# Kernel optimization log

Measured on AMD Instinct MI355X. Metric: run time of the kernel, lower is better.

## Reference

```python
import jax, jax.numpy as jnp
import numpy as np

U, I, D, OUT = 8192, 16384, 64, 64

def setup_inputs() -> dict:
    key = jax.random.key(0)
    k1, k2, k3, k4 = jax.random.split(key, 4)
    user_emb = jax.random.normal(k1, (U, D), dtype=jnp.float32)
    item_emb = jax.random.normal(k2, (I, D), dtype=jnp.float32)
    attention_weight = jax.random.normal(k3, (D, OUT), dtype=jnp.float32) * (1.0 / np.sqrt(D))
    adj_matrix = jax.random.randint(k4, (U, I), 0, 2, dtype=jnp.int32)
    return {"user_emb": user_emb, "item_emb": item_emb,
            "attention_weight": attention_weight, "adj_matrix": adj_matrix}

def reference(user_emb, item_emb, attention_weight, adj_matrix):
    # score[u,i] = <user_emb[u], item_emb[i]>  (torch.inner)
    score = jnp.einsum('ud,id->ui', user_emb, item_emb)
    # mask non-edges to 0 (NOT -inf, faithful to torch.where(adj>0, score, 0))
    score = jnp.where(adj_matrix > 0, score, 0.0)
    score = jax.nn.softmax(score, axis=1)
    # flag == True path: aggregate items into users, then project
    output = score @ item_emb          # [U, D]
    output = output @ attention_weight  # [U, OUT]
    return output
```

## Files before the change

kernel.cpp:

```cpp
#include <hip/hip_runtime.h>
#include <hip/hip_bf16.h>
#include <math.h>

#define U_N   8192
#define I_N   16384
#define D_N   64
#define OUT_N 64
#define BN    32
#define NCH   16
#define ITERS 32
#define VN_ST 72
#define VT_ST 40

typedef _Float16 half8  __attribute__((ext_vector_type(8)));
typedef short    bf16x8 __attribute__((ext_vector_type(8)));
typedef short    bf16x4 __attribute__((ext_vector_type(4)));
typedef float    f32x4  __attribute__((ext_vector_type(4)));
typedef int      int4v  __attribute__((ext_vector_type(4)));

static __device__ __forceinline__ unsigned short f2bf(float f) {
    union { __hip_bfloat16 h; unsigned short u; } cv;
    cv.h = __float2bfloat16(f);
    return cv.u;
}
static __device__ __forceinline__ void bar() {
    asm volatile("s_waitcnt lgkmcnt(0)\n\ts_barrier" ::: "memory");
}
static __device__ __forceinline__ f32x4 pv_mfma(bf16x4 a, bf16x4 b, f32x4 c) {
#if __has_builtin(__builtin_amdgcn_mfma_f32_16x16x16bf16_1k)
    return __builtin_amdgcn_mfma_f32_16x16x16bf16_1k(a, b, c, 0, 0, 0);
#else
    f32x4 d;
    asm volatile("v_mfma_f32_16x16x16_bf16 %0, %1, %2, %3"
                 : "=v"(d) : "v"(a), "v"(b), "v"(c));
    return d;
#endif
}

__global__ __launch_bounds__(256)
void prep_items(const float* __restrict__ item,
                _Float16* __restrict__ itemH,
                unsigned short* __restrict__ itemTt)
{
    const int i = blockIdx.x * 256 + threadIdx.x;
    const float* src = item + (size_t)i * D_N;
    f32x4 v[16];
    #pragma unroll
    for (int j = 0; j < 16; ++j) v[j] = *(const f32x4*)(src + 4 * j);

    #pragma unroll
    for (int j = 0; j < 8; ++j) {
        half8 h;
        #pragma unroll
        for (int k = 0; k < 4; ++k) { h[k] = (_Float16)v[2*j][k]; h[4+k] = (_Float16)v[2*j+1][k]; }
        *(half8*)&itemH[(size_t)i * D_N + 8 * j] = h;
    }
    const size_t tb = (size_t)(i >> 5) * (D_N * 32) + (i & 31);
    #pragma unroll
    for (int d = 0; d < 64; ++d)
        itemTt[tb + (size_t)d * 32] = f2bf(v[d >> 2][d & 3]);
}

#define DECL_SET(S) \
    int4v adj##S##a, adj##S##b; \
    half8 vn##S; bf16x8 vt##S;

#define LOAD_ADJ(S, tidx) do { \
    const size_t o_ = (size_t)(tidx) * BN; \
    adj##S##a = *(const int4v*)&adjq[o_];      \
    adj##S##b = *(const int4v*)&adjq[o_ + 16]; \
} while (0)

#define LOAD_TILE(S, tidx) do { \
    const size_t o_ = (size_t)(tidx) * BN; \
    vn##S = *(const half8*)&itemH[(ibase0 + o_ + (t >> 3)) * D_N + (t & 7) * 8]; \
    vt##S = *(const bf16x8*)&itemTt[((ibase0 + o_) >> 5) * (D_N * 32) \
                                    + (size_t)(t >> 2) * 32 + (t & 3) * 8]; \
} while (0)

#define COMMIT(S, bufw) do { \
    *(half8*)&Vn[bufw][(t >> 3) * VN_ST + (t & 7) * 8] = vn##S; \
    *(bf16x8*)&Vt[bufw][(t >> 2) * VT_ST + (t & 3) * 8] = vt##S; \
} while (0)

#define MASKS(S, ma, mb) \
    const unsigned ma = ((adj##S##a[0] != 0) ? 1u : 0u) | ((adj##S##a[1] != 0) ? 2u : 0u) | \
                        ((adj##S##a[2] != 0) ? 4u : 0u) | ((adj##S##a[3] != 0) ? 8u : 0u); \
    const unsigned mb = ((adj##S##b[0] != 0) ? 1u : 0u) | ((adj##S##b[1] != 0) ? 2u : 0u) | \
                        ((adj##S##b[2] != 0) ? 4u : 0u) | ((adj##S##b[3] != 0) ? 8u : 0u);

#define COMPUTE_REST(ma, mb, bufr) do { \
    half8 a00 = *(const half8*)&Vn[bufr][(c)      * VN_ST      + q * 8]; \
    half8 a01 = *(const half8*)&Vn[bufr][(c)      * VN_ST + 32 + q * 8]; \
    half8 a10 = *(const half8*)&Vn[bufr][(16 + c) * VN_ST      + q * 8]; \
    half8 a11 = *(const half8*)&Vn[bufr][(16 + c) * VN_ST + 32 + q * 8]; \
    f32x4 T0 = (f32x4){0.f,0.f,0.f,0.f}; \
    f32x4 T1 = (f32x4){0.f,0.f,0.f,0.f}; \
    T0 = __builtin_amdgcn_mfma_f32_16x16x32_f16(a00, ufrag0, T0, 0, 0, 0); \
    T0 = __builtin_amdgcn_mfma_f32_16x16x32_f16(a01, ufrag1, T0, 0, 0, 0); \
    T1 = __builtin_amdgcn_mfma_f32_16x16x32_f16(a10, ufrag0, T1, 0, 0, 0); \
    T1 = __builtin_amdgcn_mfma_f32_16x16x32_f16(a11, ufrag1, T1, 0, 0, 0); \
    bf16x4 p0, p1; \
    float e_; \
    e_ = __expf(((ma) & 1u) ? T0[0] : 0.0f); p0[0] = (short)f2bf(e_); lc += e_; \
    e_ = __expf(((ma) & 2u) ? T0[1] : 0.0f); p0[1] = (short)f2bf(e_); lc += e_; \
    e_ = __expf(((ma) & 4u) ? T0[2] : 0.0f); p0[2] = (short)f2bf(e_); lc += e_; \
    e_ = __expf(((ma) & 8u) ? T0[3] : 0.0f); p0[3] = (short)f2bf(e_); lc += e_; \
    e_ = __expf(((mb) & 1u) ? T1[0] : 0.0f); p1[0] = (short)f2bf(e_); lc += e_; \
    e_ = __expf(((mb) & 2u) ? T1[1] : 0.0f); p1[1] = (short)f2bf(e_); lc += e_; \
    e_ = __expf(((mb) & 4u) ? T1[2] : 0.0f); p1[2] = (short)f2bf(e_); lc += e_; \
    e_ = __expf(((mb) & 8u) ? T1[3] : 0.0f); p1[3] = (short)f2bf(e_); lc += e_; \
    bf16x4 vb00 = *(const bf16x4*)&Vt[bufr][(c)      * VT_ST      + 4 * q]; \
    bf16x4 vb01 = *(const bf16x4*)&Vt[bufr][(c)      * VT_ST + 16 + 4 * q]; \
    bf16x4 vb10 = *(const bf16x4*)&Vt[bufr][(16 + c) * VT_ST      + 4 * q]; \
    bf16x4 vb11 = *(const bf16x4*)&Vt[bufr][(16 + c) * VT_ST + 16 + 4 * q]; \
    bf16x4 vb20 = *(const bf16x4*)&Vt[bufr][(32 + c) * VT_ST      + 4 * q]; \
    bf16x4 vb21 = *(const bf16x4*)&Vt[bufr][(32 + c) * VT_ST + 16 + 4 * q]; \
    bf16x4 vb30 = *(const bf16x4*)&Vt[bufr][(48 + c) * VT_ST      + 4 * q]; \
    bf16x4 vb31 = *(const bf16x4*)&Vt[bufr][(48 + c) * VT_ST + 16 + 4 * q]; \
    O0 = pv_mfma(p0, vb00, O0);  O0 = pv_mfma(p1, vb01, O0); \
    O1 = pv_mfma(p0, vb10, O1);  O1 = pv_mfma(p1, vb11, O1); \
    O2 = pv_mfma(p0, vb20, O2);  O2 = pv_mfma(p1, vb21, O2); \
    O3 = pv_mfma(p0, vb30, O3);  O3 = pv_mfma(p1, vb31, O3); \
} while (0)

__global__ __launch_bounds__(256, 4)
void atten_main(const float* __restrict__ user_emb,
                const _Float16* __restrict__ itemH,
                const unsigned short* __restrict__ itemTt,
                const int*   __restrict__ adj,
                float* __restrict__ wsO,
                float* __restrict__ wsL)
{
    __shared__ _Float16 Vn[2][BN * VN_ST];
    __shared__ short    Vt[2][D_N * VT_ST];

    const int ch   = blockIdx.x;
    const int ub   = blockIdx.y;
    const int t    = threadIdx.x;
    const int w    = t >> 6;
    const int lane = t & 63;
    const int c    = lane & 15;
    const int q    = lane >> 4;

    const int    urow0  = ub * 64 + w * 16;
    const size_t ibase0 = (size_t)ch * (I_N / NCH);

    half8 ufrag0, ufrag1;
    {
        const float* up = user_emb + (size_t)(urow0 + c) * D_N + q * 8;
        f32x4 a0 = *(const f32x4*)(up);
        f32x4 b0 = *(const f32x4*)(up + 4);
        f32x4 a1 = *(const f32x4*)(up + 32);
        f32x4 b1 = *(const f32x4*)(up + 36);
        #pragma unroll
        for (int j = 0; j < 4; ++j) {
            ufrag0[j] = (_Float16)a0[j]; ufrag0[4 + j] = (_Float16)b0[j];
            ufrag1[j] = (_Float16)a1[j]; ufrag1[4 + j] = (_Float16)b1[j];
        }
    }

    f32x4 O0 = (f32x4){0.f,0.f,0.f,0.f};
    f32x4 O1 = O0, O2 = O0, O3 = O0;
    float lc = 0.f;

    const int* adjq = adj + (size_t)(urow0 + c) * I_N + ibase0 + 4 * q;

    DECL_SET(A)
    DECL_SET(B)

    LOAD_TILE(A, 0); LOAD_ADJ(A, 0);
    LOAD_TILE(B, 1); LOAD_ADJ(B, 1);
    COMMIT(A, 0);
    LOAD_TILE(A, 2);
    bar();

    for (int k = 0; k < ITERS; k += 2) {
        {
            MASKS(A, ma, mb)
            COMMIT(B, 1);
            const int ia = (k + 2 < ITERS) ? k + 2 : ITERS - 1;
            const int iv = (k + 3 < ITERS) ? k + 3 : ITERS - 1;
            LOAD_ADJ(A, ia);
            LOAD_TILE(B, iv);
            COMPUTE_REST(ma, mb, 0);
            bar();
        }
        {
            MASKS(B, ma, mb)
            COMMIT(A, 0);
            const int ia = (k + 3 < ITERS) ? k + 3 : ITERS - 1;
            const int iv = (k + 4 < ITERS) ? k + 4 : ITERS - 1;
            LOAD_ADJ(B, ia);
            LOAD_TILE(A, iv);
            COMPUTE_REST(ma, mb, 1);
            bar();
        }
    }

    lc += __shfl_xor(lc, 16);
    lc += __shfl_xor(lc, 32);

    {
        float* d0 = wsO + ((size_t)ch * U_N + urow0 + 4 * q + 0) * D_N;
        float* d1 = wsO + ((size_t)ch * U_N + urow0 + 4 * q + 1) * D_N;
        float* d2 = wsO + ((size_t)ch * U_N + urow0 + 4 * q + 2) * D_N;
        float* d3 = wsO + ((size_t)ch * U_N + urow0 + 4 * q + 3) * D_N;
        d0[c] = O0[0]; d0[16 + c] = O1[0]; d0[32 + c] = O2[0]; d0[48 + c] = O3[0];
        d1[c] = O0[1]; d1[16 + c] = O1[1]; d1[32 + c] = O2[1]; d1[48 + c] = O3[1];
        d2[c] = O0[2]; d2[16 + c] = O1[2]; d2[32 + c] = O2[2]; d2[48 + c] = O3[2];
        d3[c] = O0[3]; d3[16 + c] = O1[3]; d3[32 + c] = O2[3]; d3[48 + c] = O3[3];
    }
    if (q == 0)
        wsL[(size_t)ch * U_N + urow0 + c] = lc;
}

__global__ __launch_bounds__(256)
void atten_combine(const float* __restrict__ wsO,
                   const float* __restrict__ wsL,
                   const float* __restrict__ attw,
                   float* __restrict__ out,
                   int nch)
{
    __shared__ float inv[64];
    __shared__ float agg[64][68];
    __shared__ float Wl[64][68];

    const int t  = threadIdx.x;
    const int u0 = blockIdx.x * 64;

    {
        const int d = t >> 2, o0 = (t & 3) * 16;
        const float* src = attw + d * OUT_N + o0;
        #pragma unroll
        for (int j = 0; j < 4; ++j)
            *(f32x4*)&Wl[d][o0 + 4 * j] = *(const f32x4*)(src + 4 * j);
    }
    if (t < 64) {
        float L = 0.f;
        for (int cc = 0; cc < nch; ++cc) L += wsL[(size_t)cc * U_N + u0 + t];
        inv[t] = 1.0f / L;
    }
    __syncthreads();

    {
        const int ul = t >> 2, d0 = (t & 3) * 16;
        const int u = u0 + ul;
        f32x4 a4[4];
        #pragma unroll
        for (int j = 0; j < 4; ++j) a4[j] = (f32x4){0.f, 0.f, 0.f, 0.f};
        for (int cc = 0; cc < nch; ++cc) {
            const float* src = wsO + ((size_t)cc * U_N + u) * D_N + d0;
            #pragma unroll
            for (int j = 0; j < 4; ++j) a4[j] += *(const f32x4*)(src + 4 * j);
        }
        const float s = inv[ul];
        #pragma unroll
        for (int j = 0; j < 4; ++j)
            *(f32x4*)&agg[ul][d0 + 4 * j] = a4[j] * s;
    }
    __syncthreads();

    {
        const int ul = t >> 2, o0 = (t & 3) * 16;
        f32x4 acc[4];
        #pragma unroll
        for (int j = 0; j < 4; ++j) acc[j] = (f32x4){0.f, 0.f, 0.f, 0.f};
        for (int d = 0; d < 64; ++d) {
            const float av = agg[ul][d];
            #pragma unroll
            for (int j = 0; j < 4; ++j) {
                f32x4 wv = *(const f32x4*)&Wl[d][o0 + 4 * j];
                acc[j] += wv * av;
            }
        }
        float* dst = out + (size_t)(u0 + ul) * OUT_N + o0;
        #pragma unroll
        for (int j = 0; j < 4; ++j)
            *(f32x4*)(dst + 4 * j) = acc[j];
    }
}

extern "C" void kernel_launch(void* const* d_in, const int* in_sizes, int n_in,
                              void* d_out, int out_size, void* d_ws, size_t ws_size,
                              hipStream_t stream)
{
    const float* user_emb = (const float*)d_in[0];
    const float* item_emb = (const float*)d_in[1];
    const float* attw     = (const float*)d_in[2];
    const int*   adj      = (const int*)d_in[3];
    float* out = (float*)d_out;

    float*          wsO    = (float*)d_ws;
    float*          wsL    = wsO + (size_t)NCH * U_N * D_N;
    _Float16*       itemH  = (_Float16*)(wsL + (size_t)NCH * U_N);
    unsigned short* itemTt = (unsigned short*)(itemH + (size_t)I_N * D_N);

    prep_items<<<dim3(I_N / 256), 256, 0, stream>>>(item_emb, itemH, itemTt);
    atten_main<<<dim3(NCH, U_N / 64), 256, 0, stream>>>(user_emb, itemH, itemTt, adj,
                                                        wsO, wsL);
    atten_combine<<<dim3(U_N / 64), 256, 0, stream>>>(wsO, wsL, attw, out, NCH);
}
```

Measured before the change: 740.7 us.

## Use exp2 with prescaled user rows, truncating bf16 pack, and wider Vt reads

User fragments are prescaled by log2(e) so the softmax can use the hardware exp2 instruction directly. Probabilities are packed to bf16 by truncation with a byte-permute instead of round-to-nearest conversion. The transposed item layout is permuted so each lane reads one 16-byte Vt vector instead of two 8-byte ones. Mask bitfields are dropped in favour of reading the adj vectors directly, and the adj loads move after the compute so the registers can be reused. The item-chunk split is halved (NCH 8, more iterations per block), which halves the partial-output workspace and the reduction work but also halves the grid size.

```diff
diff --git a/kernel.cpp b/kernel.cpp
--- a/kernel.cpp
+++ b/kernel.cpp
@@ -7,8 +7,8 @@
 #define D_N   64
 #define OUT_N 64
 #define BN    32
-#define NCH   16
-#define ITERS 32
+#define NCH   8
+#define ITERS 64
 #define VN_ST 72
 #define VT_ST 40
 
@@ -22,6 +22,24 @@
     union { __hip_bfloat16 h; unsigned short u; } cv;
     cv.h = __float2bfloat16(f);
     return cv.u;
+}
+static __device__ __forceinline__ float fast_exp2(float x) {
+#if __has_builtin(__builtin_amdgcn_exp2f)
+    return __builtin_amdgcn_exp2f(x);
+#else
+    return __expf(x * 0.6931471805599453f);
+#endif
+}
+static __device__ __forceinline__ bf16x4 pack4(float a, float b, float c2, float d) {
+    union { unsigned u[2]; bf16x4 h; } x;
+#if __has_builtin(__builtin_amdgcn_perm)
+    x.u[0] = __builtin_amdgcn_perm(__float_as_uint(b), __float_as_uint(a), 0x07060302u);
+    x.u[1] = __builtin_amdgcn_perm(__float_as_uint(d), __float_as_uint(c2), 0x07060302u);
+#else
+    x.u[0] = (__float_as_uint(b) & 0xffff0000u) | (__float_as_uint(a) >> 16);
+    x.u[1] = (__float_as_uint(d) & 0xffff0000u) | (__float_as_uint(c2) >> 16);
+#endif
+    return x.h;
 }
 static __device__ __forceinline__ void bar() {
     asm volatile("s_waitcnt lgkmcnt(0)\n\ts_barrier" ::: "memory");
@@ -55,7 +73,9 @@
         for (int k = 0; k < 4; ++k) { h[k] = (_Float16)v[2*j][k]; h[4+k] = (_Float16)v[2*j+1][k]; }
         *(half8*)&itemH[(size_t)i * D_N + 8 * j] = h;
     }
-    const size_t tb = (size_t)(i >> 5) * (D_N * 32) + (i & 31);
+    const int il    = i & 31;
+    const int islot = 8 * ((il & 15) >> 2) + ((il >> 4) << 2) + (il & 3);
+    const size_t tb = (size_t)(i >> 5) * (D_N * 32) + islot;
     #pragma unroll
     for (int d = 0; d < 64; ++d)
         itemTt[tb + (size_t)d * 32] = f2bf(v[d >> 2][d & 3]);
@@ -83,45 +103,44 @@
     *(bf16x8*)&Vt[bufw][(t >> 2) * VT_ST + (t & 3) * 8] = vt##S; \
 } while (0)
 
-#define MASKS(S, ma, mb) \
-    const unsigned ma = ((adj##S##a[0] != 0) ? 1u : 0u) | ((adj##S##a[1] != 0) ? 2u : 0u) | \
-                        ((adj##S##a[2] != 0) ? 4u : 0u) | ((adj##S##a[3] != 0) ? 8u : 0u); \
-    const unsigned mb = ((adj##S##b[0] != 0) ? 1u : 0u) | ((adj##S##b[1] != 0) ? 2u : 0u) | \
-                        ((adj##S##b[2] != 0) ? 4u : 0u) | ((adj##S##b[3] != 0) ? 8u : 0u);
-
-#define COMPUTE_REST(ma, mb, bufr) do { \
+#define COMPUTE_REST(S, bufr) do { \
     half8 a00 = *(const half8*)&Vn[bufr][(c)      * VN_ST      + q * 8]; \
     half8 a01 = *(const half8*)&Vn[bufr][(c)      * VN_ST + 32 + q * 8]; \
     half8 a10 = *(const half8*)&Vn[bufr][(16 + c) * VN_ST      + q * 8]; \
     half8 a11 = *(const half8*)&Vn[bufr][(16 + c) * VN_ST + 32 + q * 8]; \
+    bf16x8 w0 = *(const bf16x8*)&Vt[bufr][(c)      * VT_ST + 8 * q]; \
+    bf16x8 w1 = *(const bf16x8*)&Vt[bufr][(16 + c) * VT_ST + 8 * q]; \
+    bf16x8 w2 = *(const bf16x8*)&Vt[bufr][(32 + c) * VT_ST + 8 * q]; \
+    bf16x8 w3 = *(const bf16x8*)&Vt[bufr][(48 + c) * VT_ST + 8 * q]; \
     f32x4 T0 = (f32x4){0.f,0.f,0.f,0.f}; \
     f32x4 T1 = (f32x4){0.f,0.f,0.f,0.f}; \
     T0 = __builtin_amdgcn_mfma_f32_16x16x32_f16(a00, ufrag0, T0, 0, 0, 0); \
     T0 = __builtin_amdgcn_mfma_f32_16x16x32_f16(a01, ufrag1, T0, 0, 0, 0); \
     T1 = __builtin_amdgcn_mfma_f32_16x16x32_f16(a10, ufrag0, T1, 0, 0, 0); \
     T1 = __builtin_amdgcn_mfma_f32_16x16x32_f16(a11, ufrag1, T1, 0, 0, 0); \
-    bf16x4 p0, p1; \
-    float e_; \
-    e_ = __expf(((ma) & 1u) ? T0[0] : 0.0f); p0[0] = (short)f2bf(e_); lc += e_; \
-    e_ = __expf(((ma) & 2u) ? T0[1] : 0.0f); p0[1] = (short)f2bf(e_); lc += e_; \
-    e_ = __expf(((ma) & 4u) ? T0[2] : 0.0f); p0[2] = (short)f2bf(e_); lc += e_; \
-    e_ = __expf(((ma) & 8u) ? T0[3] : 0.0f); p0[3] = (short)f2bf(e_); lc += e_; \
-    e_ = __expf(((mb) & 1u) ? T1[0] : 0.0f); p1[0] = (short)f2bf(e_); lc += e_; \
-    e_ = __expf(((mb) & 2u) ? T1[1] : 0.0f); p1[1] = (short)f2bf(e_); lc += e_; \
-    e_ = __expf(((mb) & 4u) ? T1[2] : 0.0f); p1[2] = (short)f2bf(e_); lc += e_; \
-    e_ = __expf(((mb) & 8u) ? T1[3] : 0.0f); p1[3] = (short)f2bf(e_); lc += e_; \
-    bf16x4 vb00 = *(const bf16x4*)&Vt[bufr][(c)      * VT_ST      + 4 * q]; \
-    bf16x4 vb01 = *(const bf16x4*)&Vt[bufr][(c)      * VT_ST + 16 + 4 * q]; \
-    bf16x4 vb10 = *(const bf16x4*)&Vt[bufr][(16 + c) * VT_ST      + 4 * q]; \
-    bf16x4 vb11 = *(const bf16x4*)&Vt[bufr][(16 + c) * VT_ST + 16 + 4 * q]; \
-    bf16x4 vb20 = *(const bf16x4*)&Vt[bufr][(32 + c) * VT_ST      + 4 * q]; \
-    bf16x4 vb21 = *(const bf16x4*)&Vt[bufr][(32 + c) * VT_ST + 16 + 4 * q]; \
-    bf16x4 vb30 = *(const bf16x4*)&Vt[bufr][(48 + c) * VT_ST      + 4 * q]; \
-    bf16x4 vb31 = *(const bf16x4*)&Vt[bufr][(48 + c) * VT_ST + 16 + 4 * q]; \
-    O0 = pv_mfma(p0, vb00, O0);  O0 = pv_mfma(p1, vb01, O0); \
-    O1 = pv_mfma(p0, vb10, O1);  O1 = pv_mfma(p1, vb11, O1); \
-    O2 = pv_mfma(p0, vb20, O2);  O2 = pv_mfma(p1, vb21, O2); \
-    O3 = pv_mfma(p0, vb30, O3);  O3 = pv_mfma(p1, vb31, O3); \
+    const float e0_ = fast_exp2((adj##S##a[0] != 0) ? T0[0] : 0.0f); \
+    const float e1_ = fast_exp2((adj##S##a[1] != 0) ? T0[1] : 0.0f); \
+    const float e2_ = fast_exp2((adj##S##a[2] != 0) ? T0[2] : 0.0f); \
+    const float e3_ = fast_exp2((adj##S##a[3] != 0) ? T0[3] : 0.0f); \
+    const float f0_ = fast_exp2((adj##S##b[0] != 0) ? T1[0] : 0.0f); \
+    const float f1_ = fast_exp2((adj##S##b[1] != 0) ? T1[1] : 0.0f); \
+    const float f2_ = fast_exp2((adj##S##b[2] != 0) ? T1[2] : 0.0f); \
+    const float f3_ = fast_exp2((adj##S##b[3] != 0) ? T1[3] : 0.0f); \
+    lc += ((e0_ + e1_) + (e2_ + e3_)) + ((f0_ + f1_) + (f2_ + f3_)); \
+    bf16x4 p0 = pack4(e0_, e1_, e2_, e3_); \
+    bf16x4 p1 = pack4(f0_, f1_, f2_, f3_); \
+    bf16x4 lo0 = __builtin_shufflevector(w0, w0, 0, 1, 2, 3); \
+    bf16x4 hi0 = __builtin_shufflevector(w0, w0, 4, 5, 6, 7); \
+    bf16x4 lo1 = __builtin_shufflevector(w1, w1, 0, 1, 2, 3); \
+    bf16x4 hi1 = __builtin_shufflevector(w1, w1, 4, 5, 6, 7); \
+    bf16x4 lo2 = __builtin_shufflevector(w2, w2, 0, 1, 2, 3); \
+    bf16x4 hi2 = __builtin_shufflevector(w2, w2, 4, 5, 6, 7); \
+    bf16x4 lo3 = __builtin_shufflevector(w3, w3, 0, 1, 2, 3); \
+    bf16x4 hi3 = __builtin_shufflevector(w3, w3, 4, 5, 6, 7); \
+    O0 = pv_mfma(p0, lo0, O0);  O0 = pv_mfma(p1, hi0, O0); \
+    O1 = pv_mfma(p0, lo1, O1);  O1 = pv_mfma(p1, hi1, O1); \
+    O2 = pv_mfma(p0, lo2, O2);  O2 = pv_mfma(p1, hi2, O2); \
+    O3 = pv_mfma(p0, lo3, O3);  O3 = pv_mfma(p1, hi3, O3); \
 } while (0)
 
 __global__ __launch_bounds__(256, 4)
@@ -149,14 +168,15 @@
     half8 ufrag0, ufrag1;
     {
         const float* up = user_emb + (size_t)(urow0 + c) * D_N + q * 8;
+        const float s = 1.44269504088896f;
         f32x4 a0 = *(const f32x4*)(up);
         f32x4 b0 = *(const f32x4*)(up + 4);
         f32x4 a1 = *(const f32x4*)(up + 32);
         f32x4 b1 = *(const f32x4*)(up + 36);
         #pragma unroll
         for (int j = 0; j < 4; ++j) {
-            ufrag0[j] = (_Float16)a0[j]; ufrag0[4 + j] = (_Float16)b0[j];
-            ufrag1[j] = (_Float16)a1[j]; ufrag1[4 + j] = (_Float16)b1[j];
+            ufrag0[j] = (_Float16)(a0[j] * s); ufrag0[4 + j] = (_Float16)(b0[j] * s);
+            ufrag1[j] = (_Float16)(a1[j] * s); ufrag1[4 + j] = (_Float16)(b1[j] * s);
         }
     }
 
@@ -177,23 +197,17 @@
 
     for (int k = 0; k < ITERS; k += 2) {
         {
-            MASKS(A, ma, mb)
             COMMIT(B, 1);
-            const int ia = (k + 2 < ITERS) ? k + 2 : ITERS - 1;
-            const int iv = (k + 3 < ITERS) ? k + 3 : ITERS - 1;
-            LOAD_ADJ(A, ia);
-            LOAD_TILE(B, iv);
-            COMPUTE_REST(ma, mb, 0);
+            LOAD_TILE(B, (k + 3 < ITERS) ? k + 3 : ITERS - 1);
+            COMPUTE_REST(A, 0);
+            LOAD_ADJ(A, (k + 2 < ITERS) ? k + 2 : ITERS - 1);
             bar();
         }
         {
-            MASKS(B, ma, mb)
             COMMIT(A, 0);
-            const int ia = (k + 3 < ITERS) ? k + 3 : ITERS - 1;
-            const int iv = (k + 4 < ITERS) ? k + 4 : ITERS - 1;
-            LOAD_ADJ(B, ia);
-            LOAD_TILE(A, iv);
-            COMPUTE_REST(ma, mb, 1);
+            LOAD_TILE(A, (k + 4 < ITERS) ? k + 4 : ITERS - 1);
+            COMPUTE_REST(B, 1);
+            LOAD_ADJ(B, (k + 3 < ITERS) ? k + 3 : ITERS - 1);
             bar();
         }
     }
```

New measurement: 728.4 us. No clear change (-1.7%).
